# Kernel tuning notes

Hardware: AMD Instinct MI355X
Metric: run time of the kernel (lower is better)

Reference implementation:

```python
import jax, jax.numpy as jnp
import numpy as np

K = 16  # neighbors

def setup_inputs() -> dict:
    key = jax.random.key(0)
    k1, k2, k3 = jax.random.split(key, 3)
    B, C_in, C_out, N = 4, 64, 64, 8192
    x = jax.random.normal(k1, (B, C_in, N), dtype=jnp.float32)
    coords = jax.random.normal(k2, (B, 3, N), dtype=jnp.float32)
    W = jax.random.normal(k3, (C_out, C_in), dtype=jnp.float32) * 0.05
    return {"x": x, "coords": coords, "W": W}


def _knn_indices(coords, k):
    # coords: [B, 3, N]; squared pairwise distances d[b,i,j] = ||c_i - c_j||^2
    sq = jnp.sum(coords * coords, axis=1)                      # [B, N]
    inner = jnp.einsum('bdi,bdj->bij', coords, coords)         # [B, N, N]
    dist = sq[:, :, None] + sq[:, None, :] - 2.0 * inner       # [B, N, N]
    # k smallest distances -> top_k of negated distances
    _, idx = jax.lax.top_k(-dist, k)                           # [B, N, k]
    return idx


def _gather_neighbors(x, idx):
    # x: [B, C, N], idx: [B, N, k] -> [B, C, N, k]
    return jax.vmap(lambda xb, ib: xb[:, ib])(x, idx)


def reference(x, coords, W):
    idx = _knn_indices(coords, K)                              # [B, N, k]
    knn_x = _gather_neighbors(x, idx)                          # [B, C_in, N, k]
    # PointwiseConv2D (1x1 conv, no bias) == channel matmul
    mlp = jnp.einsum('oc,bcnk->bonk', W, knn_x)                # [B, C_out, N, k]
    y = jnp.max(mlp, axis=-1)                                  # [B, C_out, N]
    return (y, coords)
```

## Files before the change

kernel.cpp:

```cpp
#include <hip/hip_runtime.h>

#define BB 4
#define NN 8192
#define QB 32
#define CAP 96
#define SLACK 6e-3f

typedef unsigned long long u64;
typedef unsigned int u32;
typedef _Float16 f16x8 __attribute__((ext_vector_type(8)));
typedef float f32x16 __attribute__((ext_vector_type(16)));

__device__ __forceinline__ u64 shfl_xor_u64(u64 v, int m) {
  u32 lo = (u32)v, hi = (u32)(v >> 32);
  lo = (u32)__shfl_xor((int)lo, m, 64);
  hi = (u32)__shfl_xor((int)hi, m, 64);
  return ((u64)hi << 32) | lo;
}
__device__ __forceinline__ u64 shfl_u64(u64 v, int src) {
  u32 lo = (u32)v, hi = (u32)(v >> 32);
  lo = (u32)__shfl((int)lo, src, 64);
  hi = (u32)__shfl((int)hi, src, 64);
  return ((u64)hi << 32) | lo;
}
__device__ __forceinline__ u64 min_u64(u64 a, u64 b) { return a < b ? a : b; }
__device__ __forceinline__ float rfl(float x) {
  return __int_as_float(__builtin_amdgcn_readfirstlane(__float_as_int(x)));
}

__device__ __forceinline__ u64 bitonic64(u64 v, int lane) {
#pragma unroll
  for (int k = 2; k <= 64; k <<= 1) {
#pragma unroll
    for (int jm = k >> 1; jm >= 1; jm >>= 1) {
      u64 o = shfl_xor_u64(v, jm);
      bool keepmin = ((lane & jm) == 0) == ((lane & k) == 0);
      u64 mn = min_u64(v, o);
      u64 mx = (v < o) ? o : v;
      v = keepmin ? mn : mx;
    }
  }
  return v;
}

__device__ __forceinline__ float dist_exact(float qx, float qy, float qz, float qw,
                                            float cx, float cy, float cz, float cw) {
#pragma clang fp contract(off)
  float inner = qx * cx;
  inner = inner + qy * cy;
  inner = inner + qz * cz;
  float tt = qw + cw;
  return __builtin_fmaf(-2.0f, inner, tt);
}

__global__ void fused_prep_zmat(const float* __restrict__ x, const float* __restrict__ W,
                                const float* __restrict__ coords,
                                float* __restrict__ z, float4* __restrict__ c4p,
                                _Float16* __restrict__ bfr,
                                float* __restrict__ ycoords) {
#pragma clang fp contract(off)
  __shared__ float Ws[64 * 65];
  __shared__ float xs[64 * 32];
  int t = threadIdx.x;
  if (blockIdx.x < 1024) {
    int blk = blockIdx.x;
    int b = blk >> 8;
    int j0 = (blk & 255) * 32;
    for (int r = t; r < 4096; r += 256) Ws[(r >> 6) * 65 + (r & 63)] = W[r];
    const float* xb = x + (size_t)b * 64 * NN;
    for (int r = 0; r < 8; ++r) {
      int idx = t + r * 256;
      int c = idx >> 5, j = idx & 31;
      xs[c * 32 + j] = xb[(size_t)c * NN + j0 + j];
    }
    __syncthreads();
    int o = t & 63, jb = (t >> 6) * 8;
    float acc[8];
#pragma unroll
    for (int m = 0; m < 8; ++m) acc[m] = 0.f;
    for (int c = 0; c < 64; ++c) {
      float w = Ws[o * 65 + c];
#pragma unroll
      for (int m = 0; m < 8; ++m) acc[m] = __builtin_fmaf(w, xs[c * 32 + jb + m], acc[m]);
    }
#pragma unroll
    for (int m = 0; m < 8; ++m)
      z[((size_t)b * NN + j0 + jb + m) * 64 + o] = acc[m];
  } else {
    int t2 = (blockIdx.x - 1024) * 256 + t;
    int b = t2 >> 13;
    int i = t2 & (NN - 1);
    const float* cb = coords + (size_t)b * 3 * NN;
    float cx = cb[i];
    float cy = cb[NN + i];
    float cz = cb[2 * NN + i];
    float sq = (cx * cx + cy * cy) + cz * cz;
    float4 v; v.x = -2.0f * cx; v.y = -2.0f * cy; v.z = -2.0f * cz; v.w = sq;
    c4p[t2] = v;

    _Float16 xh = (_Float16)v.x, yh = (_Float16)v.y, zh = (_Float16)v.z;
    _Float16 xl = (_Float16)(v.x - (float)xh);
    _Float16 yl = (_Float16)(v.y - (float)yh);
    _Float16 zl = (_Float16)(v.z - (float)zh);
    _Float16 sh = (_Float16)sq;
    _Float16 sl = (_Float16)(sq - (float)sh);
    f16x8 b0, b1;
    b0[0] = xh; b0[1] = xh; b0[2] = xl; b0[3] = yh;
    b0[4] = yh; b0[5] = yl; b0[6] = zh; b0[7] = zh;
    b1[0] = zl; b1[1] = sh; b1[2] = sl;
    b1[3] = (_Float16)0.f; b1[4] = (_Float16)0.f; b1[5] = (_Float16)0.f;
    b1[6] = (_Float16)0.f; b1[7] = (_Float16)0.f;
    f16x8* bp = (f16x8*)bfr;
    bp[(size_t)t2 * 2]     = b0;
    bp[(size_t)t2 * 2 + 1] = b1;

#pragma unroll
    for (int r = 0; r < 3; ++r)
      ycoords[r * (BB * NN) + t2] = coords[r * (BB * NN) + t2];
  }
}

__global__ void __launch_bounds__(256, 4) knn_gather(const float4* __restrict__ c4p,
                                                     const _Float16* __restrict__ bfr,
                                                     const float* __restrict__ z,
                                                     float* __restrict__ y) {
  __shared__ __align__(16) char pool[QB * CAP * 4];
  __shared__ float TfL[QB];
  __shared__ int scnt[QB];
  __shared__ int sidx[QB][16];
  __shared__ float ys[64][QB + 1];
  float (*wmin)[64] = (float(*)[64])pool;
  u32 (*survj)[CAP] = (u32(*)[CAP])pool;

  int t = threadIdx.x;
  int w = t >> 6, lane = t & 63;
  int lq = lane & 31, lg = lane >> 5;
  int qbase = blockIdx.x * QB;
  int b = qbase >> 13;
  int i0 = qbase & (NN - 1);
  const float4* cp = c4p + (size_t)b * NN;
  int wbase = w * (NN / 4);

  if (t < QB) scnt[t] = 0;

  float4 qv = cp[i0 + lq];
  float qx = -0.5f * qv.x, qy = -0.5f * qv.y, qz = -0.5f * qv.z;
  _Float16 xh = (_Float16)qx, yh = (_Float16)qy, zh = (_Float16)qz;
  _Float16 xl = (_Float16)(qx - (float)xh);
  _Float16 yl = (_Float16)(qy - (float)yh);
  _Float16 zl = (_Float16)(qz - (float)zh);
  f16x8 af;
  if (lg == 0) {
    af[0] = xh; af[1] = xl; af[2] = xh; af[3] = yh;
    af[4] = yl; af[5] = yh; af[6] = zh; af[7] = zl;
  } else {
    af[0] = zh; af[1] = (_Float16)1.0f; af[2] = (_Float16)1.0f;
    af[3] = (_Float16)0.f; af[4] = (_Float16)0.f; af[5] = (_Float16)0.f;
    af[6] = (_Float16)0.f; af[7] = (_Float16)0.f;
  }

  f32x16 zzz, mn;
#pragma unroll
  for (int r = 0; r < 16; ++r) { zzz[r] = 0.f; mn[r] = 3.402823466e+38f; }

  const f16x8* lp = (const f16x8*)bfr + (((size_t)b * NN + wbase + lq) * 2 + lg);

#pragma unroll 4
  for (int tt = 0; tt < 64; ++tt) {
    f16x8 bc = lp[tt * 64];
    f32x16 d = __builtin_amdgcn_mfma_f32_32x32x16_f16(af, bc, zzz, 0, 0, 0);
#pragma unroll
    for (int r = 0; r < 16; ++r) mn[r] = fminf(mn[r], d[r]);
  }

#pragma unroll
  for (int r = 0; r < 16; ++r) {
    float m2 = fminf(mn[r], __shfl_xor(mn[r], 16, 64));
    int q = (r & 3) + 8 * (r >> 2) + 4 * lg;
    if (lq < 16) wmin[q][w * 16 + lq] = m2;
  }
  __syncthreads();

#pragma unroll 1
  for (int qi = 0; qi < 8; ++qi) {
    int q = w * 8 + qi;
    float v = wmin[q][lane];
#pragma unroll
    for (int k = 2; k <= 64; k <<= 1) {
#pragma unroll
      for (int jm = k >> 1; jm >= 1; jm >>= 1) {
        float o = __shfl_xor(v, jm, 64);
        bool keepmin = ((lane & jm) == 0) == ((lane & k) == 0);
        v = keepmin ? fminf(v, o) : fmaxf(v, o);
      }
    }
    if (lane == 15) TfL[q] = v + SLACK;
  }
  __syncthreads();

  float tf[16];
#pragma unroll
  for (int r = 0; r < 16; ++r) tf[r] = TfL[(r & 3) + 8 * (r >> 2) + 4 * lg];

#pragma unroll 2
  for (int tt = 0; tt < 64; ++tt) {
    f16x8 bc = lp[tt * 64];
    f32x16 d = __builtin_amdgcn_mfma_f32_32x32x16_f16(af, bc, zzz, 0, 0, 0);
    int cand = wbase + tt * 32 + lq;
#pragma unroll
    for (int r = 0; r < 16; ++r) {
      if (d[r] <= tf[r]) {
        int q = (r & 3) + 8 * (r >> 2) + 4 * lg;
        int pos = atomicAdd(&scnt[q], 1);
        if (pos < CAP) survj[q][pos] = (u32)cand;
      }
    }
  }
  __syncthreads();

  const float* zb = z + (size_t)b * NN * 64;
#pragma unroll 1
  for (int qi = 0; qi < 8; ++qi) {
    int q = w * 8 + qi;
    int n = scnt[q]; if (n > CAP) n = CAP;
    float4 qq = cp[i0 + q];
    float eqx = rfl(-0.5f * qq.x), eqy = rfl(-0.5f * qq.y);
    float eqz = rfl(-0.5f * qq.z), eqw = rfl(qq.w);
    u64 v = ~0ull;
    if (lane < n) {
      int c = (int)survj[q][lane];
      float4 cj = cp[c];
      float de = dist_exact(eqx, eqy, eqz, eqw,
                            -0.5f * cj.x, -0.5f * cj.y, -0.5f * cj.z, cj.w);
      u32 f = __float_as_uint(de);
      u32 m32 = f ^ ((u32)(((int)f) >> 31) | 0x80000000u);
      v = ((u64)m32 << 32) | (u32)c;
    }
    v = bitonic64(v, lane);
    if (n > 64) {
      u64 v2 = ~0ull;
      if (lane + 64 < n) {
        int c = (int)survj[q][lane + 64];
        float4 cj = cp[c];
        float de = dist_exact(eqx, eqy, eqz, eqw,
                              -0.5f * cj.x, -0.5f * cj.y, -0.5f * cj.z, cj.w);
        u32 f = __float_as_uint(de);
        u32 m32 = f ^ ((u32)(((int)f) >> 31) | 0x80000000u);
        v2 = ((u64)m32 << 32) | (u32)c;
      }
      v2 = bitonic64(v2, lane);
      u64 vm = (lane < 16) ? v : ((lane < 32) ? shfl_u64(v2, lane - 16) : ~0ull);
      v = bitonic64(vm, lane);
    }
    if (lane < 16) sidx[q][lane] = (int)(v & 0xFFFFFFFFull);
  }

#pragma unroll 1
  for (int qi = 0; qi < 8; ++qi) {
    int q = w * 8 + qi;
    const int* id = sidx[q];
    float m = -3.402823466e+38f;
#pragma unroll
    for (int k = 0; k < 16; ++k)
      m = fmaxf(m, zb[(size_t)id[k] * 64 + lane]);
    ys[lane][q] = m;
  }
  __syncthreads();
#pragma unroll
  for (int r = 0; r < 8; ++r) {
    int e = r * 256 + t;
    int o = e >> 5, ql = e & 31;
    y[((size_t)b * 64 + o) * NN + i0 + ql] = ys[o][ql];
  }
}

extern "C" void kernel_launch(void* const* d_in, const int* in_sizes, int n_in,
                              void* d_out, int out_size, void* d_ws, size_t ws_size,
                              hipStream_t stream) {
  const float* x      = (const float*)d_in[0];
  const float* coords = (const float*)d_in[1];
  const float* W      = (const float*)d_in[2];
  float* y = (float*)d_out;

  char* ws = (char*)d_ws;
  float4*   c4p = (float4*)ws;
  _Float16* bfr = (_Float16*)(ws + (512u << 10));
  float*    z   = (float*)(ws + (2u << 20));

  float* ycoords = y + (size_t)BB * 64 * NN;

  fused_prep_zmat<<<1024 + 128, 256, 0, stream>>>(x, W, coords, z, c4p, bfr, ycoords);
  knn_gather<<<BB * NN / QB, 256, 0, stream>>>(c4p, bfr, z, y);
}
```

Measured before the change: 152.6 us.

## Split KNN candidate scan across eight waves per block and fold threshold into MFMA

Doubles the block to 512 threads (8 waves), so each wave scans half as many candidate points and finalizes 4 queries instead of 8. The per-wave minima buffer is widened to 128 and pairs are reduced before the bitonic threshold sort. The threshold is now passed as the negated MFMA accumulator, so the survivor test becomes a compare against zero. The first scan is unrolled to issue two MFMAs per step, and output stores are vectorized to float4. The risks are more block-level sync overhead and register pressure under launch_bounds(512,8).

Measured after the change: 137.7 us. 1.11x faster.

```diff
diff --git a/kernel.cpp b/kernel.cpp
--- a/kernel.cpp
+++ b/kernel.cpp
@@ -3,6 +3,7 @@
 #define BB 4
 #define NN 8192
 #define QB 32
+#define NW 8
 #define CAP 96
 #define SLACK 6e-3f
 
@@ -120,26 +121,27 @@
   }
 }
 
-__global__ void __launch_bounds__(256, 4) knn_gather(const float4* __restrict__ c4p,
+__global__ void __launch_bounds__(512, 8) knn_gather(const float4* __restrict__ c4p,
                                                      const _Float16* __restrict__ bfr,
                                                      const float* __restrict__ z,
                                                      float* __restrict__ y) {
-  __shared__ __align__(16) char pool[QB * CAP * 4];
+  __shared__ __align__(16) char pool[QB * 128 * 4];
   __shared__ float TfL[QB];
   __shared__ int scnt[QB];
   __shared__ int sidx[QB][16];
   __shared__ float ys[64][QB + 1];
-  float (*wmin)[64] = (float(*)[64])pool;
+  float (*wmin)[128] = (float(*)[128])pool;
   u32 (*survj)[CAP] = (u32(*)[CAP])pool;
 
   int t = threadIdx.x;
   int w = t >> 6, lane = t & 63;
   int lq = lane & 31, lg = lane >> 5;
+  int lg4 = lg << 2;
   int qbase = blockIdx.x * QB;
   int b = qbase >> 13;
   int i0 = qbase & (NN - 1);
   const float4* cp = c4p + (size_t)b * NN;
-  int wbase = w * (NN / 4);
+  int wbase = w * (NN / NW);
 
   if (t < QB) scnt[t] = 0;
 
@@ -165,26 +167,28 @@
 
   const f16x8* lp = (const f16x8*)bfr + (((size_t)b * NN + wbase + lq) * 2 + lg);
 
-#pragma unroll 4
-  for (int tt = 0; tt < 64; ++tt) {
-    f16x8 bc = lp[tt * 64];
-    f32x16 d = __builtin_amdgcn_mfma_f32_32x32x16_f16(af, bc, zzz, 0, 0, 0);
-#pragma unroll
-    for (int r = 0; r < 16; ++r) mn[r] = fminf(mn[r], d[r]);
+#pragma unroll 2
+  for (int tt = 0; tt < 32; tt += 2) {
+    f16x8 bc0 = lp[tt * 64];
+    f16x8 bc1 = lp[(tt + 1) * 64];
+    f32x16 d0 = __builtin_amdgcn_mfma_f32_32x32x16_f16(af, bc0, zzz, 0, 0, 0);
+    f32x16 d1 = __builtin_amdgcn_mfma_f32_32x32x16_f16(af, bc1, zzz, 0, 0, 0);
+#pragma unroll
+    for (int r = 0; r < 16; ++r) mn[r] = fminf(fminf(mn[r], d0[r]), d1[r]);
   }
 
 #pragma unroll
   for (int r = 0; r < 16; ++r) {
     float m2 = fminf(mn[r], __shfl_xor(mn[r], 16, 64));
-    int q = (r & 3) + 8 * (r >> 2) + 4 * lg;
+    int q = (r & 3) + 8 * (r >> 2) + lg4;
     if (lq < 16) wmin[q][w * 16 + lq] = m2;
   }
   __syncthreads();
 
 #pragma unroll 1
-  for (int qi = 0; qi < 8; ++qi) {
-    int q = w * 8 + qi;
-    float v = wmin[q][lane];
+  for (int qi = 0; qi < QB / NW; ++qi) {
+    int q = w * (QB / NW) + qi;
+    float v = fminf(wmin[q][2 * lane], wmin[q][2 * lane + 1]);
 #pragma unroll
     for (int k = 2; k <= 64; k <<= 1) {
 #pragma unroll
@@ -198,19 +202,19 @@
   }
   __syncthreads();
 
-  float tf[16];
-#pragma unroll
-  for (int r = 0; r < 16; ++r) tf[r] = TfL[(r & 3) + 8 * (r >> 2) + 4 * lg];
+  f32x16 mc;
+#pragma unroll
+  for (int r = 0; r < 16; ++r) mc[r] = -TfL[(r & 3) + 8 * (r >> 2) + lg4];
 
 #pragma unroll 2
-  for (int tt = 0; tt < 64; ++tt) {
+  for (int tt = 0; tt < 32; ++tt) {
     f16x8 bc = lp[tt * 64];
-    f32x16 d = __builtin_amdgcn_mfma_f32_32x32x16_f16(af, bc, zzz, 0, 0, 0);
+    f32x16 d = __builtin_amdgcn_mfma_f32_32x32x16_f16(af, bc, mc, 0, 0, 0);
     int cand = wbase + tt * 32 + lq;
 #pragma unroll
     for (int r = 0; r < 16; ++r) {
-      if (d[r] <= tf[r]) {
-        int q = (r & 3) + 8 * (r >> 2) + 4 * lg;
+      if (d[r] <= 0.f) {
+        int q = (r & 3) + 8 * (r >> 2) + lg4;
         int pos = atomicAdd(&scnt[q], 1);
         if (pos < CAP) survj[q][pos] = (u32)cand;
       }
@@ -220,8 +224,8 @@
 
   const float* zb = z + (size_t)b * NN * 64;
 #pragma unroll 1
-  for (int qi = 0; qi < 8; ++qi) {
-    int q = w * 8 + qi;
+  for (int qi = 0; qi < QB / NW; ++qi) {
+    int q = w * (QB / NW) + qi;
     int n = scnt[q]; if (n > CAP) n = CAP;
     float4 qq = cp[i0 + q];
     float eqx = rfl(-0.5f * qq.x), eqy = rfl(-0.5f * qq.y);
@@ -256,8 +260,8 @@
   }
 
 #pragma unroll 1
-  for (int qi = 0; qi < 8; ++qi) {
-    int q = w * 8 + qi;
+  for (int qi = 0; qi < QB / NW; ++qi) {
+    int q = w * (QB / NW) + qi;
     const int* id = sidx[q];
     float m = -3.402823466e+38f;
 #pragma unroll
@@ -266,11 +270,13 @@
     ys[lane][q] = m;
   }
   __syncthreads();
-#pragma unroll
-  for (int r = 0; r < 8; ++r) {
-    int e = r * 256 + t;
-    int o = e >> 5, ql = e & 31;
-    y[((size_t)b * 64 + o) * NN + i0 + ql] = ys[o][ql];
+  {
+    int o = t >> 3;
+    int ql0 = (t & 7) * 4;
+    float4 vv;
+    vv.x = ys[o][ql0]; vv.y = ys[o][ql0 + 1];
+    vv.z = ys[o][ql0 + 2]; vv.w = ys[o][ql0 + 3];
+    *(float4*)&y[((size_t)b * 64 + o) * NN + i0 + ql0] = vv;
   }
 }
 
@@ -290,5 +296,5 @@
   float* ycoords = y + (size_t)BB * 64 * NN;
 
   fused_prep_zmat<<<1024 + 128, 256, 0, stream>>>(x, W, coords, z, c4p, bfr, ycoords);
-  knn_gather<<<BB * NN / QB, 256, 0, stream>>>(c4p, bfr, z, y);
-}
+  knn_gather<<<BB * NN / QB, 512, 0, stream>>>(c4p, bfr, z, y);
+}
```
